# Kernel tuning notes

Measured on AMD Instinct MI355X. Metric: run time of the kernel, lower is better.

Reference implementation:

```python
import jax, jax.numpy as jnp
import numpy as np

COUNT, L1, L2, L3 = 8, 3072, 15, 32


def setup_inputs() -> dict:
    key = jax.random.key(0)
    ks = jax.random.split(key, 10)
    B = 16384
    x = jax.random.uniform(ks[0], (B, L1), dtype=jnp.float32)
    ls_indices = jax.random.randint(ks[1], (B,), 0, COUNT, dtype=jnp.int32)
    s = 1.0 / np.sqrt(L1)
    l1_w = jax.random.uniform(ks[2], (COUNT * (L2 + 1), L1), minval=-s, maxval=s, dtype=jnp.float32)
    l1_b = jax.random.uniform(ks[3], (COUNT * (L2 + 1),), minval=-s, maxval=s, dtype=jnp.float32)
    # l1_fact initialized to zero in the module; use small random values for a
    # meaningful numeric test (same math either way)
    l1f_w = 0.01 * jax.random.normal(ks[4], (L2 + 1, L1), dtype=jnp.float32)
    l1f_b = 0.01 * jax.random.normal(ks[5], (L2 + 1,), dtype=jnp.float32)
    s2 = 1.0 / np.sqrt(2 * L2)
    l2_w = jax.random.uniform(ks[6], (COUNT * L3, 2 * L2), minval=-s2, maxval=s2, dtype=jnp.float32)
    l2_b = jax.random.uniform(ks[7], (COUNT * L3,), minval=-s2, maxval=s2, dtype=jnp.float32)
    s3 = 1.0 / np.sqrt(L3)
    out_w = jax.random.uniform(ks[8], (COUNT, L3), minval=-s3, maxval=s3, dtype=jnp.float32)
    out_b = jnp.zeros((COUNT,), dtype=jnp.float32)
    return {"x": x, "ls_indices": ls_indices, "l1_w": l1_w, "l1_b": l1_b,
            "l1f_w": l1f_w, "l1f_b": l1f_b, "l2_w": l2_w, "l2_b": l2_b,
            "out_w": out_w, "out_b": out_b}


def _gather_bucket(dense, idx):
    # dense: [B, count, F]; idx: [B] -> [B, F]
    return jnp.take_along_axis(dense, idx[:, None, None], axis=1)[:, 0, :]


def reference(x, ls_indices, l1_w, l1_b, l1f_w, l1f_b, l2_w, l2_b, out_w, out_b):
    B = x.shape[0]
    idx = ls_indices.reshape(-1)
    # L1 stage: dense over all buckets, then gather selected bucket
    l1s = (x @ l1_w.T + l1_b).reshape(B, COUNT, L2 + 1)
    l1c = _gather_bucket(l1s, idx)                      # [B, L2+1]
    l1f = x @ l1f_w.T + l1f_b                           # [B, L2+1]
    l1c_main, l1c_out = l1c[:, :L2], l1c[:, L2:]
    l1f_main, l1f_out = l1f[:, :L2], l1f[:, L2:]
    l1x = l1c_main + l1f_main
    # squared-clipped-ReLU pair: [x^2 * 127/128, x] clamped to [0,1]
    l1x = jnp.clip(jnp.concatenate([jnp.square(l1x) * (127.0 / 128.0), l1x], axis=1), 0.0, 1.0)
    # L2 stage
    l2s = (l1x @ l2_w.T + l2_b).reshape(B, COUNT, L3)
    l2x = jnp.clip(_gather_bucket(l2s, idx), 0.0, 1.0)  # [B, L3]
    # output stage
    l3s = (l2x @ out_w.T + out_b).reshape(B, COUNT, 1)
    l3c = _gather_bucket(l3s, idx)                      # [B, 1]
    return l3c + l1f_out + l1c_out
```

## Files before the change

kernel.cpp:

```cpp
#include <hip/hip_runtime.h>
#include <stdint.h>

#define CNT 8
#define L1D 3072
#define NB 16384
#define BM 32
#define BN 128
#define KITERS 48

typedef float  float4v  __attribute__((ext_vector_type(4)));
typedef short  short8   __attribute__((ext_vector_type(8)));

__device__ __forceinline__ unsigned short f2bf(float f) {
  uint32_t u = __builtin_bit_cast(uint32_t, f);
  u += 0x7fffu + ((u >> 16) & 1u);
  return (unsigned short)(u >> 16);
}

__global__ void prep_kernel(const float* __restrict__ l1w, const float* __restrict__ l1b,
                            const float* __restrict__ l1fw, const float* __restrict__ l1fb,
                            unsigned short* __restrict__ cw, float* __restrict__ cb) {
  const int n = blockIdx.y;
  const int k = blockIdx.x * 256 + threadIdx.x;
  const unsigned short v = f2bf(l1w[n * L1D + k] + l1fw[(n & 15) * L1D + k]);
  const int kk  = k >> 5;
  const int sub = (k >> 3) & 3;
  const int e   = k & 7;
  const int lane = sub * 16 + (n & 15);
  cw[(((n >> 4) * 96 + kk) * 64 + lane) * 8 + e] = v;
  if (blockIdx.x == 0 && n == 0 && threadIdx.x < 128)
    cb[threadIdx.x] = l1b[threadIdx.x] + l1fb[threadIdx.x & 15];
}

struct __align__(16) EpSMem {
  float yg[BM][20];
  float l2w[960 * 9];
  float outw[256];
  float l2b[256];
  float bias[128];
  int   buck[BM];
};

__global__ __launch_bounds__(256, 2) void fused_kernel(
    const float* __restrict__ x, const int* __restrict__ lsi,
    const unsigned short* __restrict__ cw, const float* __restrict__ cb,
    const float* __restrict__ gl2w, const float* __restrict__ gl2b,
    const float* __restrict__ goutw, const float* __restrict__ goutb,
    float* __restrict__ out) {
  __shared__ EpSMem sm;
  const int tid  = threadIdx.x;
  const int lane = tid & 63;
  const int wid  = tid >> 6;
  const int rowbase = blockIdx.x * BM;

  const int r16 = lane & 15;
  const int kc  = lane >> 4;

  const float* aPtr0 = x + (size_t)(rowbase + 0 * 16 + r16) * L1D + kc * 8;
  const float* aPtr1 = x + (size_t)(rowbase + 1 * 16 + r16) * L1D + kc * 8;
  const unsigned short* bPtr0 = cw + (size_t)(2 * wid + 0) * (96 * 512) + lane * 8;
  const unsigned short* bPtr1 = cw + (size_t)(2 * wid + 1) * (96 * 512) + lane * 8;

  float4v acc[2][2];
#pragma unroll
  for (int i = 0; i < 2; ++i)
#pragma unroll
    for (int j = 0; j < 2; ++j) acc[i][j] = float4v{0.f, 0.f, 0.f, 0.f};

  struct Buf { float4v a[8]; short8 b[4]; };
  Buf b0, b1, b2;

#define LOADBUF(B_, IT_)                                                              \
  {                                                                                   \
    const int koff = (IT_) * 64;                                                      \
    _Pragma("unroll")                                                                 \
    for (int ks = 0; ks < 2; ++ks) {                                                  \
      _Pragma("unroll")                                                               \
      for (int h = 0; h < 2; ++h) {                                                   \
        (B_).a[(0 * 2 + ks) * 2 + h] = *(const float4v*)(aPtr0 + koff + ks * 32 + h * 4); \
        (B_).a[(1 * 2 + ks) * 2 + h] = *(const float4v*)(aPtr1 + koff + ks * 32 + h * 4); \
      }                                                                               \
      (B_).b[0 * 2 + ks] = *(const short8*)(bPtr0 + ((IT_) * 2 + ks) * 512);          \
      (B_).b[1 * 2 + ks] = *(const short8*)(bPtr1 + ((IT_) * 2 + ks) * 512);          \
    }                                                                                 \
  }

#define COMPUTEBUF(B_)                                                                \
  {                                                                                   \
    _Pragma("unroll")                                                                 \
    for (int ks = 0; ks < 2; ++ks) {                                                  \
      short8 afr[2];                                                                  \
      _Pragma("unroll")                                                               \
      for (int i = 0; i < 2; ++i) {                                                   \
        const float4v lo = (B_).a[(i * 2 + ks) * 2 + 0];                              \
        const float4v hi = (B_).a[(i * 2 + ks) * 2 + 1];                              \
        afr[i] = short8{(short)f2bf(lo.x), (short)f2bf(lo.y), (short)f2bf(lo.z),      \
                        (short)f2bf(lo.w), (short)f2bf(hi.x), (short)f2bf(hi.y),      \
                        (short)f2bf(hi.z), (short)f2bf(hi.w)};                        \
      }                                                                               \
      _Pragma("unroll")                                                               \
      for (int i = 0; i < 2; ++i)                                                     \
        _Pragma("unroll")                                                             \
        for (int j = 0; j < 2; ++j)                                                   \
          acc[i][j] = __builtin_amdgcn_mfma_f32_16x16x32_bf16(afr[i], (B_).b[j * 2 + ks], \
                                                              acc[i][j], 0, 0, 0);    \
    }                                                                                 \
  }

  LOADBUF(b0, 0);
  LOADBUF(b1, 1);
  LOADBUF(b2, 2);
  for (int it = 0; it < KITERS; it += 3) {
    COMPUTEBUF(b0); if (it + 3 < KITERS) LOADBUF(b0, it + 3);
    COMPUTEBUF(b1); if (it + 4 < KITERS) LOADBUF(b1, it + 4);
    COMPUTEBUF(b2); if (it + 5 < KITERS) LOADBUF(b2, it + 5);
    if (it == 12 || it == 24 || it == 36)
      __builtin_amdgcn_s_barrier();
  }
#undef LOADBUF
#undef COMPUTEBUF

  if (tid < BM)  sm.buck[tid] = lsi[rowbase + tid];
  if (tid < 128) sm.bias[tid] = cb[tid];
  {
    const int b2 = tid >> 5, n2 = tid & 31;
    sm.outw[n2 * 8 + b2] = goutw[tid];
    sm.l2b[tid] = gl2b[tid];
  }
  for (int i = tid; i < 960 * 8; i += 256) {
    const int b = i / 960;
    const int rem = i - b * 960;
    sm.l2w[rem * 9 + b] = gl2w[i];
  }
  __syncthreads();

#pragma unroll
  for (int i = 0; i < 2; ++i)
#pragma unroll
    for (int j = 0; j < 2; ++j) {
      const int nt = wid * 2 + j;
#pragma unroll
      for (int rg = 0; rg < 4; ++rg) {
        const int r = i * 16 + (lane >> 4) * 4 + rg;
        if (sm.buck[r] == nt) sm.yg[r][lane & 15] = acc[i][j][rg];
      }
    }
  __syncthreads();

  {
    const int r = tid >> 3, q = tid & 7;
    const int b = sm.buck[r];
    float act[30];
#pragma unroll
    for (int c = 0; c < 15; ++c) {
      const float v = sm.yg[r][c] + sm.bias[b * 16 + c];
      act[c]      = fminf(v * v * (127.0f / 128.0f), 1.0f);
      act[15 + c] = fminf(fmaxf(v, 0.0f), 1.0f);
    }
    const float y15 = sm.yg[r][15] + sm.bias[b * 16 + 15];
    float o = 0.0f;
#pragma unroll
    for (int nn = 0; nn < 4; ++nn) {
      const int n = q * 4 + nn;
      float s = sm.l2b[b * 32 + n];
#pragma unroll
      for (int k = 0; k < 30; ++k) s += act[k] * sm.l2w[(n * 30 + k) * 9 + b];
      s = fminf(fmaxf(s, 0.0f), 1.0f);
      o += s * sm.outw[n * 8 + b];
    }
    o += __shfl_down(o, 4, 8);
    o += __shfl_down(o, 2, 8);
    o += __shfl_down(o, 1, 8);
    if (q == 0) out[rowbase + r] = o + y15 + goutb[b];
  }
}

extern "C" void kernel_launch(void* const* d_in, const int* in_sizes, int n_in,
                              void* d_out, int out_size, void* d_ws, size_t ws_size,
                              hipStream_t stream) {
  const float* x    = (const float*)d_in[0];
  const int*   lsi  = (const int*)d_in[1];
  const float* l1w  = (const float*)d_in[2];
  const float* l1b  = (const float*)d_in[3];
  const float* l1fw = (const float*)d_in[4];
  const float* l1fb = (const float*)d_in[5];
  const float* l2w  = (const float*)d_in[6];
  const float* l2b  = (const float*)d_in[7];
  const float* outw = (const float*)d_in[8];
  const float* outb = (const float*)d_in[9];
  float* out = (float*)d_out;

  unsigned short* cw = (unsigned short*)d_ws;
  float* cb = (float*)((char*)d_ws + 128 * L1D * sizeof(unsigned short));

  prep_kernel<<<dim3(12, 128), 256, 0, stream>>>(l1w, l1b, l1fw, l1fb, cw, cb);
  fused_kernel<<<NB / BM, 256, 0, stream>>>(x, lsi, cw, cb, l2w, l2b, outw, outb, out);
}
```

Before: 345.0 us.

## Sort rows by bucket and compute only the selected bucket's L1 columns

Adds a scatter kernel that groups row indices by bucket with atomics. The fused kernel then runs per bucket chunk and computes only that bucket's 16 L1 outputs instead of all 128. Operands are staged into LDS with direct global-to-LDS loads and swizzling, and K is split across wave pairs whose partial sums are added in the epilogue. This removes the redundant dense matmul over unused buckets, at the cost of an extra launch, gathered row access, and roughly half the blocks exiting early.

```diff
diff --git a/kernel.cpp b/kernel.cpp
--- a/kernel.cpp
+++ b/kernel.cpp
@@ -1,12 +1,9 @@
 #include <hip/hip_runtime.h>
 #include <stdint.h>
 
-#define CNT 8
 #define L1D 3072
 #define NB 16384
-#define BM 32
-#define BN 128
-#define KITERS 48
+#define CAP 4096
 
 typedef float  float4v  __attribute__((ext_vector_type(4)));
 typedef short  short8   __attribute__((ext_vector_type(8)));
@@ -17,9 +14,15 @@
   return (unsigned short)(u >> 16);
 }
 
+__device__ __forceinline__ void gload_lds16(const void* g, void* l) {
+  __builtin_amdgcn_global_load_lds((const __attribute__((address_space(1))) unsigned int*)g,
+                                   (__attribute__((address_space(3))) unsigned int*)l, 16, 0, 0);
+}
+
 __global__ void prep_kernel(const float* __restrict__ l1w, const float* __restrict__ l1b,
                             const float* __restrict__ l1fw, const float* __restrict__ l1fb,
-                            unsigned short* __restrict__ cw, float* __restrict__ cb) {
+                            unsigned short* __restrict__ cw, float* __restrict__ cb,
+                            int* __restrict__ cur) {
   const int n = blockIdx.y;
   const int k = blockIdx.x * 256 + threadIdx.x;
   const unsigned short v = f2bf(l1w[n * L1D + k] + l1fw[(n & 15) * L1D + k]);
@@ -30,148 +33,154 @@
   cw[(((n >> 4) * 96 + kk) * 64 + lane) * 8 + e] = v;
   if (blockIdx.x == 0 && n == 0 && threadIdx.x < 128)
     cb[threadIdx.x] = l1b[threadIdx.x] + l1fb[threadIdx.x & 15];
-}
-
-struct __align__(16) EpSMem {
-  float yg[BM][20];
-  float l2w[960 * 9];
-  float outw[256];
-  float l2b[256];
-  float bias[128];
-  int   buck[BM];
+  if (blockIdx.x == 0 && n == 0 && threadIdx.x < 8) cur[threadIdx.x] = 0;
+}
+
+__global__ void scatter_kernel(const int* __restrict__ lsi, int* __restrict__ cur,
+                               int* __restrict__ sorted) {
+  const int i = blockIdx.x * 256 + threadIdx.x;
+  const int b = lsi[i];
+  const int pos = atomicAdd(&cur[b], 1);
+  sorted[b * CAP + pos] = i;
+}
+
+struct __align__(16) EpS {
+  float ygp[2][32][20];
+  float l2wb[960];
+  float outwb[32];
+  float l2bb[32];
+  float biasb[16];
+  int   rows[32];
 };
 
-__global__ __launch_bounds__(256, 2) void fused_kernel(
-    const float* __restrict__ x, const int* __restrict__ lsi,
-    const unsigned short* __restrict__ cw, const float* __restrict__ cb,
+union __align__(16) SMem {
+  struct { char slab[4][2][6144]; } st;
+  EpS ep;
+};
+
+__global__ __launch_bounds__(256, 3) void fused_kernel(
+    const float* __restrict__ x, const unsigned short* __restrict__ cw,
+    const float* __restrict__ cb,
     const float* __restrict__ gl2w, const float* __restrict__ gl2b,
     const float* __restrict__ goutw, const float* __restrict__ goutb,
+    const int* __restrict__ cur, const int* __restrict__ sorted,
     float* __restrict__ out) {
-  __shared__ EpSMem sm;
+  __shared__ SMem sm;
   const int tid  = threadIdx.x;
   const int lane = tid & 63;
   const int wid  = tid >> 6;
-  const int rowbase = blockIdx.x * BM;
-
-  const int r16 = lane & 15;
-  const int kc  = lane >> 4;
-
-  const float* aPtr0 = x + (size_t)(rowbase + 0 * 16 + r16) * L1D + kc * 8;
-  const float* aPtr1 = x + (size_t)(rowbase + 1 * 16 + r16) * L1D + kc * 8;
-  const unsigned short* bPtr0 = cw + (size_t)(2 * wid + 0) * (96 * 512) + lane * 8;
-  const unsigned short* bPtr1 = cw + (size_t)(2 * wid + 1) * (96 * 512) + lane * 8;
-
-  float4v acc[2][2];
-#pragma unroll
-  for (int i = 0; i < 2; ++i)
-#pragma unroll
-    for (int j = 0; j < 2; ++j) acc[i][j] = float4v{0.f, 0.f, 0.f, 0.f};
-
-  struct Buf { float4v a[8]; short8 b[4]; };
-  Buf b0, b1, b2;
-
-#define LOADBUF(B_, IT_)                                                              \
-  {                                                                                   \
-    const int koff = (IT_) * 64;                                                      \
-    _Pragma("unroll")                                                                 \
-    for (int ks = 0; ks < 2; ++ks) {                                                  \
-      _Pragma("unroll")                                                               \
-      for (int h = 0; h < 2; ++h) {                                                   \
-        (B_).a[(0 * 2 + ks) * 2 + h] = *(const float4v*)(aPtr0 + koff + ks * 32 + h * 4); \
-        (B_).a[(1 * 2 + ks) * 2 + h] = *(const float4v*)(aPtr1 + koff + ks * 32 + h * 4); \
-      }                                                                               \
-      (B_).b[0 * 2 + ks] = *(const short8*)(bPtr0 + ((IT_) * 2 + ks) * 512);          \
-      (B_).b[1 * 2 + ks] = *(const short8*)(bPtr1 + ((IT_) * 2 + ks) * 512);          \
-    }                                                                                 \
-  }
-
-#define COMPUTEBUF(B_)                                                                \
-  {                                                                                   \
-    _Pragma("unroll")                                                                 \
-    for (int ks = 0; ks < 2; ++ks) {                                                  \
-      short8 afr[2];                                                                  \
-      _Pragma("unroll")                                                               \
-      for (int i = 0; i < 2; ++i) {                                                   \
-        const float4v lo = (B_).a[(i * 2 + ks) * 2 + 0];                              \
-        const float4v hi = (B_).a[(i * 2 + ks) * 2 + 1];                              \
-        afr[i] = short8{(short)f2bf(lo.x), (short)f2bf(lo.y), (short)f2bf(lo.z),      \
-                        (short)f2bf(lo.w), (short)f2bf(hi.x), (short)f2bf(hi.y),      \
-                        (short)f2bf(hi.z), (short)f2bf(hi.w)};                        \
-      }                                                                               \
-      _Pragma("unroll")                                                               \
-      for (int i = 0; i < 2; ++i)                                                     \
-        _Pragma("unroll")                                                             \
-        for (int j = 0; j < 2; ++j)                                                   \
-          acc[i][j] = __builtin_amdgcn_mfma_f32_16x16x32_bf16(afr[i], (B_).b[j * 2 + ks], \
-                                                              acc[i][j], 0, 0, 0);    \
-    }                                                                                 \
-  }
-
-  LOADBUF(b0, 0);
-  LOADBUF(b1, 1);
-  LOADBUF(b2, 2);
-  for (int it = 0; it < KITERS; it += 3) {
-    COMPUTEBUF(b0); if (it + 3 < KITERS) LOADBUF(b0, it + 3);
-    COMPUTEBUF(b1); if (it + 4 < KITERS) LOADBUF(b1, it + 4);
-    COMPUTEBUF(b2); if (it + 5 < KITERS) LOADBUF(b2, it + 5);
-    if (it == 12 || it == 24 || it == 36)
-      __builtin_amdgcn_s_barrier();
-  }
-#undef LOADBUF
-#undef COMPUTEBUF
-
-  if (tid < BM)  sm.buck[tid] = lsi[rowbase + tid];
-  if (tid < 128) sm.bias[tid] = cb[tid];
-  {
-    const int b2 = tid >> 5, n2 = tid & 31;
-    sm.outw[n2 * 8 + b2] = goutw[tid];
-    sm.l2b[tid] = gl2b[tid];
-  }
-  for (int i = tid; i < 960 * 8; i += 256) {
-    const int b = i / 960;
-    const int rem = i - b * 960;
-    sm.l2w[rem * 9 + b] = gl2w[i];
-  }
+  const int bucket = blockIdx.x >> 7;
+  const int chunk  = blockIdx.x & 127;
+  const int count  = cur[bucket];
+  const int start  = chunk * 32;
+  if (start >= count) return;
+
+  const int h = wid >> 1;
+  const int p = wid & 1;
+
+  const char* aP[4];
+#pragma unroll
+  for (int q = 0; q < 4; ++q) {
+    const int lr = q * 4 + (lane >> 4);
+    int sr = start + h * 16 + lr;
+    sr = (sr < count) ? sr : (count - 1);
+    const int grow = sorted[bucket * CAP + sr];
+    const int co = ((lane & 15) * 16) ^ ((lr & 7) << 4);
+    aP[q] = (const char*)x + (size_t)grow * (L1D * 4) + co;
+  }
+  const char* bP = (const char*)cw + ((size_t)bucket * 96 * 64 + lane) * 16;
+  char* slab = (char*)sm.st.slab[wid];
+
+  float4v acc = {0.f, 0.f, 0.f, 0.f};
+
+#define STAGE(BUF_, T_)                                                        \
+  {                                                                            \
+    char* d_ = slab + (BUF_) * 6144;                                           \
+    _Pragma("unroll")                                                          \
+    for (int q = 0; q < 4; ++q)                                                \
+      gload_lds16(aP[q] + (T_) * 256, d_ + q * 1024);                          \
+    _Pragma("unroll")                                                          \
+    for (int ks = 0; ks < 2; ++ks)                                             \
+      gload_lds16(bP + (size_t)((T_) * 2 + ks) * 1024, d_ + 4096 + ks * 1024); \
+  }
+
+#define BODY(BUF_, DOSTAGE_, NT_)                                              \
+  {                                                                            \
+    const char* base_ = slab + (BUF_) * 6144;                                  \
+    const int r_ = lane & 15, sw_ = (r_ & 7) << 4;                             \
+    short8 afr[2], bfr[2];                                                     \
+    _Pragma("unroll")                                                          \
+    for (int ks = 0; ks < 2; ++ks) {                                           \
+      const int G_ = ks * 128 + (lane >> 4) * 32;                              \
+      const float4v lo = *(const float4v*)(base_ + r_ * 256 + (G_ ^ sw_));     \
+      const float4v hi = *(const float4v*)(base_ + r_ * 256 + ((G_ + 16) ^ sw_)); \
+      afr[ks] = short8{(short)f2bf(lo.x), (short)f2bf(lo.y), (short)f2bf(lo.z),\
+                       (short)f2bf(lo.w), (short)f2bf(hi.x), (short)f2bf(hi.y),\
+                       (short)f2bf(hi.z), (short)f2bf(hi.w)};                  \
+      bfr[ks] = *(const short8*)(base_ + 4096 + ks * 1024 + lane * 16);        \
+    }                                                                          \
+    asm volatile("" ::: "memory");      \
+    if (DOSTAGE_) STAGE(BUF_, NT_)                                             \
+    _Pragma("unroll")                                                          \
+    for (int ks = 0; ks < 2; ++ks)                                             \
+      acc = __builtin_amdgcn_mfma_f32_16x16x32_bf16(afr[ks], bfr[ks], acc, 0, 0, 0); \
+  }
+
+  STAGE(0, p)
+  STAGE(1, p + 2)
+
+#pragma unroll 2
+  for (int idx = 0; idx < 22; ++idx) {
+    asm volatile("s_waitcnt vmcnt(6)" ::: "memory");
+    BODY(idx & 1, 1, 2 * (idx + 2) + p)
+  }
+  asm volatile("s_waitcnt vmcnt(6)" ::: "memory");
+  BODY(0, 0, 0)
+  asm volatile("s_waitcnt vmcnt(0)" ::: "memory");
+  BODY(1, 0, 0)
+#undef STAGE
+#undef BODY
+
   __syncthreads();
 
-#pragma unroll
-  for (int i = 0; i < 2; ++i)
-#pragma unroll
-    for (int j = 0; j < 2; ++j) {
-      const int nt = wid * 2 + j;
-#pragma unroll
-      for (int rg = 0; rg < 4; ++rg) {
-        const int r = i * 16 + (lane >> 4) * 4 + rg;
-        if (sm.buck[r] == nt) sm.yg[r][lane & 15] = acc[i][j][rg];
-      }
-    }
+  if (tid < 32) {
+    const int sr = start + tid;
+    sm.ep.rows[tid]  = (sr < count) ? sorted[bucket * CAP + sr] : -1;
+    sm.ep.outwb[tid] = goutw[bucket * 32 + tid];
+    sm.ep.l2bb[tid]  = gl2b[bucket * 32 + tid];
+  }
+  if (tid < 16) sm.ep.biasb[tid] = cb[bucket * 16 + tid];
+  for (int i = tid; i < 960; i += 256) sm.ep.l2wb[i] = gl2w[bucket * 960 + i];
+#pragma unroll
+  for (int rg = 0; rg < 4; ++rg)
+    sm.ep.ygp[p][h * 16 + (lane >> 4) * 4 + rg][lane & 15] = acc[rg];
   __syncthreads();
 
   {
     const int r = tid >> 3, q = tid & 7;
-    const int b = sm.buck[r];
+    const int grow = sm.ep.rows[r];
     float act[30];
 #pragma unroll
     for (int c = 0; c < 15; ++c) {
-      const float v = sm.yg[r][c] + sm.bias[b * 16 + c];
+      const float v = sm.ep.ygp[0][r][c] + sm.ep.ygp[1][r][c] + sm.ep.biasb[c];
       act[c]      = fminf(v * v * (127.0f / 128.0f), 1.0f);
       act[15 + c] = fminf(fmaxf(v, 0.0f), 1.0f);
     }
-    const float y15 = sm.yg[r][15] + sm.bias[b * 16 + 15];
+    const float y15 = sm.ep.ygp[0][r][15] + sm.ep.ygp[1][r][15] + sm.ep.biasb[15];
     float o = 0.0f;
 #pragma unroll
     for (int nn = 0; nn < 4; ++nn) {
       const int n = q * 4 + nn;
-      float s = sm.l2b[b * 32 + n];
-#pragma unroll
-      for (int k = 0; k < 30; ++k) s += act[k] * sm.l2w[(n * 30 + k) * 9 + b];
+      float s = sm.ep.l2bb[n];
+#pragma unroll
+      for (int k = 0; k < 30; ++k) s += act[k] * sm.ep.l2wb[n * 30 + k];
       s = fminf(fmaxf(s, 0.0f), 1.0f);
-      o += s * sm.outw[n * 8 + b];
+      o += s * sm.ep.outwb[n];
     }
     o += __shfl_down(o, 4, 8);
     o += __shfl_down(o, 2, 8);
     o += __shfl_down(o, 1, 8);
-    if (q == 0) out[rowbase + r] = o + y15 + goutb[b];
+    if (q == 0 && grow >= 0) out[grow] = o + y15 + goutb[bucket];
   }
 }
 
@@ -191,8 +200,12 @@
   float* out = (float*)d_out;
 
   unsigned short* cw = (unsigned short*)d_ws;
-  float* cb = (float*)((char*)d_ws + 128 * L1D * sizeof(unsigned short));
-
-  prep_kernel<<<dim3(12, 128), 256, 0, stream>>>(l1w, l1b, l1fw, l1fb, cw, cb);
-  fused_kernel<<<NB / BM, 256, 0, stream>>>(x, lsi, cw, cb, l2w, l2b, outw, outb, out);
-}
+  float* cb   = (float*)((char*)d_ws + 786432);
+  int*   cur  = (int*)  ((char*)d_ws + 786944);
+  int*   sorted = (int*)((char*)d_ws + 786976);
+
+  prep_kernel<<<dim3(12, 128), 256, 0, stream>>>(l1w, l1b, l1fw, l1fb, cw, cb, cur);
+  scatter_kernel<<<NB / 256, 256, 0, stream>>>(lsi, cur, sorted);
+  fused_kernel<<<8 * (CAP / 32), 256, 0, stream>>>(x, cw, cb, l2w, l2b, outw, outb,
+                                                   cur, sorted, out);
+}
```

Result: slower. 365.1 us (+5.8%).
